# Performance work log

Measured on AMD Instinct MI355X. Metric: run time of the kernel, lower is better.

The kernel has to match this reference:

```python
import jax, jax.numpy as jnp
import numpy as np

T = 8192  # context/question length (input_shape[2])
D = 128   # feature dim (input_shape[3])


def setup_inputs() -> dict:
    key = jax.random.key(0)
    k1, k2 = jax.random.split(key)
    x = jax.random.normal(k1, (2, 1, T, D), dtype=jnp.float32)
    kernel = jax.random.normal(k2, (3 * D,), dtype=jnp.float32)
    return {"x": x, "kernel": kernel}


def reference(x, kernel):
    context = x[0, 0]   # (T, D)
    question = x[1, 0]  # (T, D)
    w_c, w_q, w_m = kernel[:D], kernel[D:2 * D], kernel[2 * D:]

    # Additive similarity: S[i,j] = c_i.w_c + q_j.w_q + (c_i*q_j).w_m
    # Avoids materializing the (T, T, 3D) tiled/concatenated tensor.
    S = (context @ w_c)[:, None] + (question @ w_q)[None, :] \
        + (context * w_m) @ question.T  # (T, T)

    A = jax.nn.softmax(S, axis=-1)  # row-wise softmax, as tf.nn.softmax on 2D

    # C2Q attention: U_A[i] = sum_j A[i,j] * q_j
    U_A = A @ question  # (T, D)

    # Q2C attention: b = row-max of A, h = sum_i b_i * c_i, tiled over rows
    b = jnp.max(A, axis=1)          # (T,)
    h = b @ context                 # (D,)
    H_A = jnp.broadcast_to(h, (T, D))

    # megamerge: [c, U_A, c*U_A, c*H_A]
    G = jnp.concatenate([context, U_A, context * U_A, context * H_A], axis=-1)
    return G  # (T, 4D)
```

## Files before the change

### kernel.cpp

```cpp
#include <hip/hip_runtime.h>
#include <hip/hip_bf16.h>

#define T 8192
#define D 128
#define NSPLIT 8
#define JLEN (T / NSPLIT)
#define BN 64
#define NITER (JLEN / BN)
#define BM 128
#define LOG2E 1.44269504088896f

typedef _Float16 half4_t __attribute__((ext_vector_type(4)));
typedef _Float16 half8_t __attribute__((ext_vector_type(8)));
typedef float floatx4 __attribute__((ext_vector_type(4)));

__global__ void prep_kernel(const float* __restrict__ x, const float* __restrict__ kern,
                            _Float16* __restrict__ q16, _Float16* __restrict__ qT16,
                            _Float16* __restrict__ cm16, float* __restrict__ qq2) {
    const float* context  = x;
    const float* question = x + (size_t)T * D;
    const float* wq = kern + D;
    const float* wm = kern + 2 * D;
    __shared__ __align__(16) _Float16 tile[32][136];
    int j0 = blockIdx.x * 32;
    int t = threadIdx.x;
    int c4 = t & 31;
    int rsub = t >> 5;
    float4 wqv = ((const float4*)wq)[c4];
    float4 wmv = ((const float4*)wm)[c4];
    for (int p = 0; p < 4; ++p) {
        int row = p * 8 + rsub;
        float4 q = ((const float4*)(question + (size_t)(j0 + row) * D))[c4];
        float4 c = ((const float4*)(context  + (size_t)(j0 + row) * D))[c4];
        half4_t qh;
        qh[0] = (_Float16)q.x; qh[1] = (_Float16)q.y; qh[2] = (_Float16)q.z; qh[3] = (_Float16)q.w;
        *(half4_t*)(q16 + (size_t)(j0 + row) * D + c4 * 4) = qh;
        *(half4_t*)&tile[row][c4 * 4] = qh;
        half4_t ch;
        ch[0] = (_Float16)(c.x * wmv.x * LOG2E); ch[1] = (_Float16)(c.y * wmv.y * LOG2E);
        ch[2] = (_Float16)(c.z * wmv.z * LOG2E); ch[3] = (_Float16)(c.w * wmv.w * LOG2E);
        *(half4_t*)(cm16 + (size_t)(j0 + row) * D + c4 * 4) = ch;
        float s = q.x * wqv.x + q.y * wqv.y + q.z * wqv.z + q.w * wqv.w;
        for (int dx = 1; dx <= 16; dx <<= 1) s += __shfl_xor(s, dx);
        if (c4 == 0) qq2[j0 + row] = s * LOG2E;
    }
    __syncthreads();
    for (int p = 0; p < 2; ++p) {
        int chunk = t + p * 256;
        int d = chunk >> 2, jo = (chunk & 3) * 8;
        half8_t v;
        for (int s2 = 0; s2 < 8; ++s2) v[s2] = tile[jo + s2][d];
        *(half8_t*)(qT16 + (size_t)d * T + j0 + jo) = v;
    }
}

__global__ __launch_bounds__(256, 2)
void flash_kernel(const _Float16* __restrict__ q16, const _Float16* __restrict__ qT16,
                  const _Float16* __restrict__ cm16, const float* __restrict__ qq2,
                  unsigned char* __restrict__ Opart, float* __restrict__ mpart,
                  float* __restrict__ lpart) {
    __shared__ __align__(16) _Float16 Kt[64][144];
    __shared__ __align__(16) _Float16 Vt[128][72];
    __shared__ __align__(16) float qqs[JLEN];

    int bx = blockIdx.x;
    int rb = bx >> 3;
    int sp = bx & 7;
    int tid = threadIdx.x;
    int wave = tid >> 6;
    int lane = tid & 63;
    int quad = lane >> 4;
    int l15 = lane & 15;
    int rbase = rb * BM + wave * 32;

    ((float4*)qqs)[tid] = ((const float4*)(qq2 + (size_t)sp * JLEN))[tid];

    half8_t qfrag[2][4];
    for (int mt = 0; mt < 2; ++mt)
        for (int ks = 0; ks < 4; ++ks)
            qfrag[mt][ks] = *(const half8_t*)(cm16 + (size_t)(rbase + mt * 16 + l15) * D
                                              + ks * 32 + quad * 8);

    floatx4 acc[2][8];
    for (int mt = 0; mt < 2; ++mt)
        for (int nt = 0; nt < 8; ++nt)
            for (int r = 0; r < 4; ++r) acc[mt][nt][r] = 0.f;
    float m_run[2] = {-INFINITY, -INFINITY};
    float l_run[2] = {0.f, 0.f};

    half8_t kreg[4], vreg[4];
    {
        int j0 = sp * JLEN;
        for (int k = 0; k < 4; ++k) {
            int idx = tid + k * 256;
            kreg[k] = *(const half8_t*)(q16 + (size_t)(j0 + (idx >> 4)) * D + (idx & 15) * 8);
            vreg[k] = *(const half8_t*)(qT16 + (size_t)(idx >> 3) * T + j0 + (idx & 7) * 8);
        }
    }

    for (int it = 0; it < NITER; ++it) {
        for (int k = 0; k < 4; ++k) {
            int idx = tid + k * 256;
            *(half8_t*)&Kt[idx >> 4][(idx & 15) * 8] = kreg[k];
        }
        for (int k = 0; k < 4; ++k) {
            int idx = tid + k * 256;
            int dr = idx >> 3, c8 = idx & 7;
            int ph0 = (c8 >> 2) * 32 + (c8 & 1) * 16 + ((c8 >> 1) & 1) * 4;
            half4_t lo, hi;
            lo[0] = vreg[k][0]; lo[1] = vreg[k][1]; lo[2] = vreg[k][2]; lo[3] = vreg[k][3];
            hi[0] = vreg[k][4]; hi[1] = vreg[k][5]; hi[2] = vreg[k][6]; hi[3] = vreg[k][7];
            *(half4_t*)&Vt[dr][ph0]     = lo;
            *(half4_t*)&Vt[dr][ph0 + 8] = hi;
        }
        __syncthreads();

        if (it + 1 < NITER) {
            int j0n = sp * JLEN + (it + 1) * BN;
            for (int k = 0; k < 4; ++k) {
                int idx = tid + k * 256;
                kreg[k] = *(const half8_t*)(q16 + (size_t)(j0n + (idx >> 4)) * D + (idx & 15) * 8);
                vreg[k] = *(const half8_t*)(qT16 + (size_t)(idx >> 3) * T + j0n + (idx & 7) * 8);
            }
        }

        floatx4 St[2][4];
        for (int jt = 0; jt < 4; ++jt) {
            float4 bias = *(const float4*)&qqs[it * 64 + jt * 16 + quad * 4];
            St[0][jt][0] = bias.x; St[0][jt][1] = bias.y; St[0][jt][2] = bias.z; St[0][jt][3] = bias.w;
            St[1][jt][0] = bias.x; St[1][jt][1] = bias.y; St[1][jt][2] = bias.z; St[1][jt][3] = bias.w;
        }
        for (int ks = 0; ks < 4; ++ks)
            for (int jt = 0; jt < 4; ++jt) {
                half8_t a = *(const half8_t*)&Kt[jt * 16 + l15][ks * 32 + quad * 8];
                St[0][jt] = __builtin_amdgcn_mfma_f32_16x16x32_f16(a, qfrag[0][ks], St[0][jt], 0, 0, 0);
                St[1][jt] = __builtin_amdgcn_mfma_f32_16x16x32_f16(a, qfrag[1][ks], St[1][jt], 0, 0, 0);
            }

        half4_t apv[2][4];
        float alpha[2];
        for (int mt = 0; mt < 2; ++mt) {
            float mx = St[mt][0][0];
            for (int jt = 0; jt < 4; ++jt)
                for (int r = 0; r < 4; ++r) mx = fmaxf(mx, St[mt][jt][r]);
            mx = fmaxf(mx, __shfl_xor(mx, 16));
            mx = fmaxf(mx, __shfl_xor(mx, 32));
            float mnew = fmaxf(m_run[mt], mx);
            alpha[mt] = __builtin_amdgcn_exp2f(m_run[mt] - mnew);
            m_run[mt] = mnew;
            float ps = 0.f;
            for (int jt = 0; jt < 4; ++jt) {
                float p0 = __builtin_amdgcn_exp2f(St[mt][jt][0] - mnew);
                float p1 = __builtin_amdgcn_exp2f(St[mt][jt][1] - mnew);
                float p2 = __builtin_amdgcn_exp2f(St[mt][jt][2] - mnew);
                float p3 = __builtin_amdgcn_exp2f(St[mt][jt][3] - mnew);
                ps += (p0 + p1) + (p2 + p3);
                apv[mt][jt][0] = (_Float16)p0;
                apv[mt][jt][1] = (_Float16)p1;
                apv[mt][jt][2] = (_Float16)p2;
                apv[mt][jt][3] = (_Float16)p3;
            }
            ps += __shfl_xor(ps, 16);
            ps += __shfl_xor(ps, 32);
            l_run[mt] = l_run[mt] * alpha[mt] + ps;
        }
        for (int mt = 0; mt < 2; ++mt) {
            float aT[4];
            for (int r = 0; r < 4; ++r)
                aT[r] = __shfl(alpha[mt], quad * 4 + r);
            for (int nt = 0; nt < 8; ++nt)
                for (int r = 0; r < 4; ++r) acc[mt][nt][r] *= aT[r];
        }

        for (int pr = 0; pr < 2; ++pr) {
            for (int nt = 0; nt < 8; ++nt) {
                half8_t bb = *(const half8_t*)&Vt[nt * 16 + l15][pr * 32 + quad * 8];
                half4_t b0, b1;
                b0[0] = bb[0]; b0[1] = bb[1]; b0[2] = bb[2]; b0[3] = bb[3];
                b1[0] = bb[4]; b1[1] = bb[5]; b1[2] = bb[6]; b1[3] = bb[7];
                int jt0 = pr * 2, jt1 = pr * 2 + 1;
                acc[0][nt] = __builtin_amdgcn_mfma_f32_16x16x16f16(apv[0][jt0], b0, acc[0][nt], 0, 0, 0);
                acc[1][nt] = __builtin_amdgcn_mfma_f32_16x16x16f16(apv[1][jt0], b0, acc[1][nt], 0, 0, 0);
                acc[0][nt] = __builtin_amdgcn_mfma_f32_16x16x16f16(apv[0][jt1], b1, acc[0][nt], 0, 0, 0);
                acc[1][nt] = __builtin_amdgcn_mfma_f32_16x16x16f16(apv[1][jt1], b1, acc[1][nt], 0, 0, 0);
            }
        }
        __syncthreads();
    }

    for (int mt = 0; mt < 2; ++mt) {
        if (quad == 0) {
            int iq = rbase + mt * 16 + l15;
            mpart[(size_t)sp * T + iq] = m_run[mt];
            lpart[(size_t)sp * T + iq] = l_run[mt];
        }
        float rinv[4];
        for (int r = 0; r < 4; ++r)
            rinv[r] = 1.0f / __shfl(l_run[mt], quad * 4 + r);
        int i = rbase + mt * 16 + quad * 4;
        for (int nt = 0; nt < 4; ++nt)
            ;
        for (int nt = 0; nt < 8; ++nt) {
            for (int r = 0; r < 4; r += 2) {
                float v0 = acc[mt][nt][r]     * rinv[r];
                float v1 = acc[mt][nt][r + 1] * rinv[r + 1];
                int p0 = __builtin_amdgcn_cvt_pk_fp8_f32(v0, v0, 0, false);
                int p1 = __builtin_amdgcn_cvt_pk_fp8_f32(v1, v1, 0, false);
                Opart[((size_t)sp * T + (i + r))     * D + nt * 16 + l15] = (unsigned char)(p0 & 0xFF);
                Opart[((size_t)sp * T + (i + r + 1)) * D + nt * 16 + l15] = (unsigned char)(p1 & 0xFF);
            }
        }
    }
}

__global__ void merge_kernel(const unsigned char* __restrict__ Opart, const float* __restrict__ mpart,
                             const float* __restrict__ lpart, float* __restrict__ U_A,
                             float* __restrict__ linv) {
    int t = threadIdx.x;
    int i = blockIdx.x * 16 + (t >> 4);
    int c = t & 15;
    float mp[NSPLIT];
    float mstar = -INFINITY;
    for (int sp = 0; sp < NSPLIT; ++sp) {
        mp[sp] = mpart[(size_t)sp * T + i];
        mstar = fmaxf(mstar, mp[sp]);
    }
    float L = 0.f;
    float u[8];
    for (int k = 0; k < 8; ++k) u[k] = 0.f;
    int d0 = c * 8;
    for (int sp = 0; sp < NSPLIT; ++sp) {
        float w = __builtin_amdgcn_exp2f(mp[sp] - mstar) * lpart[(size_t)sp * T + i];
        L += w;
        uint2 ow = *(const uint2*)(Opart + ((size_t)sp * T + i) * D + d0);
        u[0] += __builtin_amdgcn_cvt_f32_fp8(ow.x, 0) * w;
        u[1] += __builtin_amdgcn_cvt_f32_fp8(ow.x, 1) * w;
        u[2] += __builtin_amdgcn_cvt_f32_fp8(ow.x, 2) * w;
        u[3] += __builtin_amdgcn_cvt_f32_fp8(ow.x, 3) * w;
        u[4] += __builtin_amdgcn_cvt_f32_fp8(ow.y, 0) * w;
        u[5] += __builtin_amdgcn_cvt_f32_fp8(ow.y, 1) * w;
        u[6] += __builtin_amdgcn_cvt_f32_fp8(ow.y, 2) * w;
        u[7] += __builtin_amdgcn_cvt_f32_fp8(ow.y, 3) * w;
    }
    float invL = 1.0f / L;
    float4 s0 = make_float4(u[0] * invL, u[1] * invL, u[2] * invL, u[3] * invL);
    float4 s1 = make_float4(u[4] * invL, u[5] * invL, u[6] * invL, u[7] * invL);
    *(float4*)(U_A + (size_t)i * D + d0) = s0;
    *(float4*)(U_A + (size_t)i * D + d0 + 4) = s1;
    if (c == 0) linv[i] = invL;
}

__global__ void hsum_part_kernel(const float* __restrict__ x, const float* __restrict__ linv,
                                 float* __restrict__ hpart) {
    const float* context = x;
    int t = threadIdx.x;
    int d = t & 127, g = t >> 7;
    int i0 = blockIdx.x * 128 + g * 64;
    float s = 0.f;
    for (int k = 0; k < 64; ++k)
        s += context[(size_t)(i0 + k) * D + d] * linv[i0 + k];
    hpart[(size_t)(blockIdx.x * 2 + g) * 128 + d] = s;
}

__global__ void hreduce_kernel(const float* __restrict__ hpart, float* __restrict__ h) {
    int d = threadIdx.x;
    float s = 0.f;
    for (int k = 0; k < 128; ++k) s += hpart[(size_t)k * 128 + d];
    h[d] = s;
}

__global__ void assemble_kernel(const float* __restrict__ x, const float* __restrict__ U_A,
                                const float* __restrict__ h, float* __restrict__ out) {
    const float* context = x;
    int gid = blockIdx.x * 256 + threadIdx.x;
    int base = gid * 4;
    int i = base >> 9;
    int c = base & 511;
    int seg = c >> 7, d = c & 127;
    float4 r;
    if (seg == 0) {
        r = *(const float4*)(context + (size_t)i * D + d);
    } else if (seg == 1) {
        r = *(const float4*)(U_A + (size_t)i * D + d);
    } else if (seg == 2) {
        float4 a = *(const float4*)(context + (size_t)i * D + d);
        float4 b = *(const float4*)(U_A + (size_t)i * D + d);
        r = make_float4(a.x * b.x, a.y * b.y, a.z * b.z, a.w * b.w);
    } else {
        float4 a = *(const float4*)(context + (size_t)i * D + d);
        float4 b = *(const float4*)(h + d);
        r = make_float4(a.x * b.x, a.y * b.y, a.z * b.z, a.w * b.w);
    }
    *(float4*)(out + base) = r;
}

extern "C" void kernel_launch(void* const* d_in, const int* in_sizes, int n_in,
                              void* d_out, int out_size, void* d_ws, size_t ws_size,
                              hipStream_t stream) {
    const float* x = (const float*)d_in[0];
    const float* kern = (const float*)d_in[1];
    float* out = (float*)d_out;

    char* w = (char*)d_ws;
    size_t off = 0;
    _Float16* q16  = (_Float16*)(w + off); off += (size_t)T * D * 2;
    _Float16* qT16 = (_Float16*)(w + off); off += (size_t)T * D * 2;
    _Float16* cm16 = (_Float16*)(w + off); off += (size_t)T * D * 2;
    float* qq2   = (float*)(w + off); off += (size_t)T * 4;
    float* mpart = (float*)(w + off); off += (size_t)NSPLIT * T * 4;
    float* lpart = (float*)(w + off); off += (size_t)NSPLIT * T * 4;
    float* U_A   = (float*)(w + off); off += (size_t)T * D * 4;
    float* linv  = (float*)(w + off); off += (size_t)T * 4;
    float* hpart = (float*)(w + off); off += (size_t)128 * 128 * 4;
    float* h     = (float*)(w + off); off += (size_t)D * 4;

    unsigned char* Opart = (unsigned char*)d_out;

    prep_kernel<<<256, 256, 0, stream>>>(x, kern, q16, qT16, cm16, qq2);
    flash_kernel<<<512, 256, 0, stream>>>(q16, qT16, cm16, qq2, Opart, mpart, lpart);
    merge_kernel<<<512, 256, 0, stream>>>(Opart, mpart, lpart, U_A, linv);
    hsum_part_kernel<<<64, 256, 0, stream>>>(x, linv, hpart);
    hreduce_kernel<<<1, 128, 0, stream>>>(hpart, h);
    assemble_kernel<<<4096, 256, 0, stream>>>(x, U_A, h, out);
}
```

Before: 131.7 us.

## Rework flash kernel with 32x32 MFMA, double-buffered LDS, and fused reduction kernels

The flash attention kernel moves from 16x16 MFMA tiles to 32x32x16 MFMA with one 32-row tile per wave. K and V now sit in double-buffered LDS with an XOR-style swizzle for V, prefetched two iterations ahead, so there is one barrier per iteration. It also adds lazy rescaling (skipped when no row max grows), packed fp16 conversion and setprio hints. On the host side, the h reduction is restructured: a new combine kernel computes the inverse softmax normalisers straight from the per-split m and l values, and merge folds in the final h reduce, cutting one launch. The risk is more register pressure from the 16-wide accumulators and mistakes in the new lane mapping.

```diff
diff --git a/kernel.cpp b/kernel.cpp
--- a/kernel.cpp
+++ b/kernel.cpp
@@ -10,9 +10,12 @@
 #define BM 128
 #define LOG2E 1.44269504088896f
 
+typedef _Float16 half2_t __attribute__((ext_vector_type(2)));
 typedef _Float16 half4_t __attribute__((ext_vector_type(4)));
 typedef _Float16 half8_t __attribute__((ext_vector_type(8)));
+typedef __fp16 fp16x2_t __attribute__((ext_vector_type(2)));
 typedef float floatx4 __attribute__((ext_vector_type(4)));
+typedef float floatx16 __attribute__((ext_vector_type(16)));
 
 __global__ void prep_kernel(const float* __restrict__ x, const float* __restrict__ kern,
                             _Float16* __restrict__ q16, _Float16* __restrict__ qT16,
@@ -59,164 +62,207 @@
                   const _Float16* __restrict__ cm16, const float* __restrict__ qq2,
                   unsigned char* __restrict__ Opart, float* __restrict__ mpart,
                   float* __restrict__ lpart) {
-    __shared__ __align__(16) _Float16 Kt[64][144];
-    __shared__ __align__(16) _Float16 Vt[128][72];
+    __shared__ __align__(16) _Float16 Kt[2][64][136];
+    __shared__ __align__(16) _Float16 Vt[2][128][64];
     __shared__ __align__(16) float qqs[JLEN];
 
-    int bx = blockIdx.x;
-    int rb = bx >> 3;
-    int sp = bx & 7;
-    int tid = threadIdx.x;
-    int wave = tid >> 6;
-    int lane = tid & 63;
-    int quad = lane >> 4;
-    int l15 = lane & 15;
-    int rbase = rb * BM + wave * 32;
+    const int bx = blockIdx.x;
+    const int rb = bx >> 3;
+    const int sp = bx & 7;
+    const int tid = threadIdx.x;
+    const int wave = tid >> 6;
+    const int lane = tid & 63;
+    const int l31 = lane & 31;
+    const int h = lane >> 5;
+    const int rbase = rb * BM + wave * 32;
+    const int q = rbase + l31;
+    const int sig = (l31 & 19) | ((l31 & 4) << 1) | ((l31 & 8) >> 1);
 
     ((float4*)qqs)[tid] = ((const float4*)(qq2 + (size_t)sp * JLEN))[tid];
 
-    half8_t qfrag[2][4];
-    for (int mt = 0; mt < 2; ++mt)
-        for (int ks = 0; ks < 4; ++ks)
-            qfrag[mt][ks] = *(const half8_t*)(cm16 + (size_t)(rbase + mt * 16 + l15) * D
-                                              + ks * 32 + quad * 8);
-
-    floatx4 acc[2][8];
-    for (int mt = 0; mt < 2; ++mt)
-        for (int nt = 0; nt < 8; ++nt)
-            for (int r = 0; r < 4; ++r) acc[mt][nt][r] = 0.f;
-    float m_run[2] = {-INFINITY, -INFINITY};
-    float l_run[2] = {0.f, 0.f};
-
+    half8_t qfrag[8];
+#pragma unroll
+    for (int ks = 0; ks < 8; ++ks)
+        qfrag[ks] = *(const half8_t*)(cm16 + (size_t)q * D + ks * 16 + h * 8);
+
+    floatx16 acc[4];
+#pragma unroll
+    for (int nt = 0; nt < 4; ++nt)
+#pragma unroll
+        for (int r = 0; r < 16; ++r) acc[nt][r] = 0.f;
+    float m_run = -INFINITY, l_run = 0.f;
+
+    const int j0 = sp * JLEN;
     half8_t kreg[4], vreg[4];
-    {
-        int j0 = sp * JLEN;
-        for (int k = 0; k < 4; ++k) {
-            int idx = tid + k * 256;
-            kreg[k] = *(const half8_t*)(q16 + (size_t)(j0 + (idx >> 4)) * D + (idx & 15) * 8);
-            vreg[k] = *(const half8_t*)(qT16 + (size_t)(idx >> 3) * T + j0 + (idx & 7) * 8);
-        }
-    }
+#pragma unroll
+    for (int k = 0; k < 4; ++k) {
+        int idx = tid + k * 256;
+        kreg[k] = *(const half8_t*)(q16 + (size_t)(j0 + (idx >> 4)) * D + (idx & 15) * 8);
+        vreg[k] = *(const half8_t*)(qT16 + (size_t)(idx >> 3) * T + j0 + (idx & 7) * 8);
+    }
+#pragma unroll
+    for (int k = 0; k < 4; ++k) {
+        int idx = tid + k * 256;
+        *(half8_t*)&Kt[0][idx >> 4][(idx & 15) * 8] = kreg[k];
+        int dr = idx >> 3, c8 = idx & 7;
+        *(half8_t*)&Vt[0][dr][((c8 + (dr & 7)) & 7) * 8] = vreg[k];
+    }
+#pragma unroll
+    for (int k = 0; k < 4; ++k) {
+        int idx = tid + k * 256;
+        kreg[k] = *(const half8_t*)(q16 + (size_t)(j0 + BN + (idx >> 4)) * D + (idx & 15) * 8);
+        vreg[k] = *(const half8_t*)(qT16 + (size_t)(idx >> 3) * T + j0 + BN + (idx & 7) * 8);
+    }
+    __syncthreads();
 
     for (int it = 0; it < NITER; ++it) {
-        for (int k = 0; k < 4; ++k) {
-            int idx = tid + k * 256;
-            *(half8_t*)&Kt[idx >> 4][(idx & 15) * 8] = kreg[k];
-        }
-        for (int k = 0; k < 4; ++k) {
-            int idx = tid + k * 256;
-            int dr = idx >> 3, c8 = idx & 7;
-            int ph0 = (c8 >> 2) * 32 + (c8 & 1) * 16 + ((c8 >> 1) & 1) * 4;
-            half4_t lo, hi;
-            lo[0] = vreg[k][0]; lo[1] = vreg[k][1]; lo[2] = vreg[k][2]; lo[3] = vreg[k][3];
-            hi[0] = vreg[k][4]; hi[1] = vreg[k][5]; hi[2] = vreg[k][6]; hi[3] = vreg[k][7];
-            *(half4_t*)&Vt[dr][ph0]     = lo;
-            *(half4_t*)&Vt[dr][ph0 + 8] = hi;
-        }
-        __syncthreads();
-
+        const int cur = it & 1;
         if (it + 1 < NITER) {
-            int j0n = sp * JLEN + (it + 1) * BN;
+#pragma unroll
             for (int k = 0; k < 4; ++k) {
                 int idx = tid + k * 256;
-                kreg[k] = *(const half8_t*)(q16 + (size_t)(j0n + (idx >> 4)) * D + (idx & 15) * 8);
-                vreg[k] = *(const half8_t*)(qT16 + (size_t)(idx >> 3) * T + j0n + (idx & 7) * 8);
-            }
-        }
-
-        floatx4 St[2][4];
-        for (int jt = 0; jt < 4; ++jt) {
-            float4 bias = *(const float4*)&qqs[it * 64 + jt * 16 + quad * 4];
-            St[0][jt][0] = bias.x; St[0][jt][1] = bias.y; St[0][jt][2] = bias.z; St[0][jt][3] = bias.w;
-            St[1][jt][0] = bias.x; St[1][jt][1] = bias.y; St[1][jt][2] = bias.z; St[1][jt][3] = bias.w;
-        }
-        for (int ks = 0; ks < 4; ++ks)
-            for (int jt = 0; jt < 4; ++jt) {
-                half8_t a = *(const half8_t*)&Kt[jt * 16 + l15][ks * 32 + quad * 8];
-                St[0][jt] = __builtin_amdgcn_mfma_f32_16x16x32_f16(a, qfrag[0][ks], St[0][jt], 0, 0, 0);
-                St[1][jt] = __builtin_amdgcn_mfma_f32_16x16x32_f16(a, qfrag[1][ks], St[1][jt], 0, 0, 0);
-            }
-
-        half4_t apv[2][4];
-        float alpha[2];
-        for (int mt = 0; mt < 2; ++mt) {
-            float mx = St[mt][0][0];
-            for (int jt = 0; jt < 4; ++jt)
-                for (int r = 0; r < 4; ++r) mx = fmaxf(mx, St[mt][jt][r]);
-            mx = fmaxf(mx, __shfl_xor(mx, 16));
-            mx = fmaxf(mx, __shfl_xor(mx, 32));
-            float mnew = fmaxf(m_run[mt], mx);
-            alpha[mt] = __builtin_amdgcn_exp2f(m_run[mt] - mnew);
-            m_run[mt] = mnew;
-            float ps = 0.f;
-            for (int jt = 0; jt < 4; ++jt) {
-                float p0 = __builtin_amdgcn_exp2f(St[mt][jt][0] - mnew);
-                float p1 = __builtin_amdgcn_exp2f(St[mt][jt][1] - mnew);
-                float p2 = __builtin_amdgcn_exp2f(St[mt][jt][2] - mnew);
-                float p3 = __builtin_amdgcn_exp2f(St[mt][jt][3] - mnew);
-                ps += (p0 + p1) + (p2 + p3);
-                apv[mt][jt][0] = (_Float16)p0;
-                apv[mt][jt][1] = (_Float16)p1;
-                apv[mt][jt][2] = (_Float16)p2;
-                apv[mt][jt][3] = (_Float16)p3;
-            }
-            ps += __shfl_xor(ps, 16);
-            ps += __shfl_xor(ps, 32);
-            l_run[mt] = l_run[mt] * alpha[mt] + ps;
-        }
-        for (int mt = 0; mt < 2; ++mt) {
-            float aT[4];
-            for (int r = 0; r < 4; ++r)
-                aT[r] = __shfl(alpha[mt], quad * 4 + r);
-            for (int nt = 0; nt < 8; ++nt)
-                for (int r = 0; r < 4; ++r) acc[mt][nt][r] *= aT[r];
-        }
-
-        for (int pr = 0; pr < 2; ++pr) {
-            for (int nt = 0; nt < 8; ++nt) {
-                half8_t bb = *(const half8_t*)&Vt[nt * 16 + l15][pr * 32 + quad * 8];
-                half4_t b0, b1;
-                b0[0] = bb[0]; b0[1] = bb[1]; b0[2] = bb[2]; b0[3] = bb[3];
-                b1[0] = bb[4]; b1[1] = bb[5]; b1[2] = bb[6]; b1[3] = bb[7];
-                int jt0 = pr * 2, jt1 = pr * 2 + 1;
-                acc[0][nt] = __builtin_amdgcn_mfma_f32_16x16x16f16(apv[0][jt0], b0, acc[0][nt], 0, 0, 0);
-                acc[1][nt] = __builtin_amdgcn_mfma_f32_16x16x16f16(apv[1][jt0], b0, acc[1][nt], 0, 0, 0);
-                acc[0][nt] = __builtin_amdgcn_mfma_f32_16x16x16f16(apv[0][jt1], b1, acc[0][nt], 0, 0, 0);
-                acc[1][nt] = __builtin_amdgcn_mfma_f32_16x16x16f16(apv[1][jt1], b1, acc[1][nt], 0, 0, 0);
-            }
-        }
+                *(half8_t*)&Kt[cur ^ 1][idx >> 4][(idx & 15) * 8] = kreg[k];
+                int dr = idx >> 3, c8 = idx & 7;
+                *(half8_t*)&Vt[cur ^ 1][dr][((c8 + (dr & 7)) & 7) * 8] = vreg[k];
+            }
+        }
+        if (it + 2 < NITER) {
+            int jn = j0 + (it + 2) * BN;
+#pragma unroll
+            for (int k = 0; k < 4; ++k) {
+                int idx = tid + k * 256;
+                kreg[k] = *(const half8_t*)(q16 + (size_t)(jn + (idx >> 4)) * D + (idx & 15) * 8);
+                vreg[k] = *(const half8_t*)(qT16 + (size_t)(idx >> 3) * T + jn + (idx & 7) * 8);
+            }
+        }
+
+        floatx16 St[2];
+#pragma unroll
+        for (int jt = 0; jt < 2; ++jt) {
+            const float* qb = &qqs[it * 64 + jt * 32];
+            float4 b0 = *(const float4*)(qb + 8 * h);
+            float4 b1 = *(const float4*)(qb + 4 + 8 * h);
+            float4 b2 = *(const float4*)(qb + 16 + 8 * h);
+            float4 b3 = *(const float4*)(qb + 20 + 8 * h);
+            St[jt][0]  = b0.x; St[jt][1]  = b0.y; St[jt][2]  = b0.z; St[jt][3]  = b0.w;
+            St[jt][4]  = b1.x; St[jt][5]  = b1.y; St[jt][6]  = b1.z; St[jt][7]  = b1.w;
+            St[jt][8]  = b2.x; St[jt][9]  = b2.y; St[jt][10] = b2.z; St[jt][11] = b2.w;
+            St[jt][12] = b3.x; St[jt][13] = b3.y; St[jt][14] = b3.z; St[jt][15] = b3.w;
+            __builtin_amdgcn_s_setprio(1);
+#pragma unroll
+            for (int ks = 0; ks < 8; ++ks) {
+                half8_t a = *(const half8_t*)&Kt[cur][jt * 32 + sig][ks * 16 + h * 8];
+                St[jt] = __builtin_amdgcn_mfma_f32_32x32x16_f16(a, qfrag[ks], St[jt], 0, 0, 0);
+            }
+            __builtin_amdgcn_s_setprio(0);
+        }
+
+        float mx = St[0][0];
+#pragma unroll
+        for (int r = 1; r < 16; ++r) mx = fmaxf(mx, St[0][r]);
+#pragma unroll
+        for (int r = 0; r < 16; ++r) mx = fmaxf(mx, St[1][r]);
+        mx = fmaxf(mx, __shfl_xor(mx, 32));
+        if (__any(mx > m_run)) {
+            float mnew = fmaxf(m_run, mx);
+            float alpha = __builtin_amdgcn_exp2f(m_run - mnew);
+#pragma unroll
+            for (int nt = 0; nt < 4; ++nt)
+#pragma unroll
+                for (int r = 0; r < 16; ++r) acc[nt][r] *= alpha;
+            l_run *= alpha;
+            m_run = mnew;
+        }
+        half2_t pp[2][8];
+        float ps = 0.f;
+#pragma unroll
+        for (int jt = 0; jt < 2; ++jt)
+#pragma unroll
+            for (int r2 = 0; r2 < 8; ++r2) {
+                float p0 = __builtin_amdgcn_exp2f(St[jt][2 * r2]     - m_run);
+                float p1 = __builtin_amdgcn_exp2f(St[jt][2 * r2 + 1] - m_run);
+                ps += p0 + p1;
+                fp16x2_t pk = __builtin_amdgcn_cvt_pkrtz(p0, p1);
+                pp[jt][r2] = __builtin_bit_cast(half2_t, pk);
+            }
+        ps += __shfl_xor(ps, 32);
+        l_run += ps;
+
+        __builtin_amdgcn_s_setprio(1);
+#pragma unroll
+        for (int jt = 0; jt < 2; ++jt)
+#pragma unroll
+            for (int kb = 0; kb < 2; ++kb) {
+                half8_t pb;
+                pb[0] = pp[jt][kb * 4 + 0][0]; pb[1] = pp[jt][kb * 4 + 0][1];
+                pb[2] = pp[jt][kb * 4 + 1][0]; pb[3] = pp[jt][kb * 4 + 1][1];
+                pb[4] = pp[jt][kb * 4 + 2][0]; pb[5] = pp[jt][kb * 4 + 2][1];
+                pb[6] = pp[jt][kb * 4 + 3][0]; pb[7] = pp[jt][kb * 4 + 3][1];
+                const int pg = ((jt * 4 + kb * 2 + h) + (l31 & 7)) & 7;
+#pragma unroll
+                for (int nt = 0; nt < 4; ++nt) {
+                    half8_t va = *(const half8_t*)&Vt[cur][nt * 32 + l31][pg * 8];
+                    acc[nt] = __builtin_amdgcn_mfma_f32_32x32x16_f16(va, pb, acc[nt], 0, 0, 0);
+                }
+            }
+        __builtin_amdgcn_s_setprio(0);
         __syncthreads();
     }
 
-    for (int mt = 0; mt < 2; ++mt) {
-        if (quad == 0) {
-            int iq = rbase + mt * 16 + l15;
-            mpart[(size_t)sp * T + iq] = m_run[mt];
-            lpart[(size_t)sp * T + iq] = l_run[mt];
-        }
-        float rinv[4];
-        for (int r = 0; r < 4; ++r)
-            rinv[r] = 1.0f / __shfl(l_run[mt], quad * 4 + r);
-        int i = rbase + mt * 16 + quad * 4;
-        for (int nt = 0; nt < 4; ++nt)
-            ;
-        for (int nt = 0; nt < 8; ++nt) {
-            for (int r = 0; r < 4; r += 2) {
-                float v0 = acc[mt][nt][r]     * rinv[r];
-                float v1 = acc[mt][nt][r + 1] * rinv[r + 1];
-                int p0 = __builtin_amdgcn_cvt_pk_fp8_f32(v0, v0, 0, false);
-                int p1 = __builtin_amdgcn_cvt_pk_fp8_f32(v1, v1, 0, false);
-                Opart[((size_t)sp * T + (i + r))     * D + nt * 16 + l15] = (unsigned char)(p0 & 0xFF);
-                Opart[((size_t)sp * T + (i + r + 1)) * D + nt * 16 + l15] = (unsigned char)(p1 & 0xFF);
-            }
-        }
-    }
+    if (h == 0) {
+        mpart[(size_t)sp * T + q] = m_run;
+        lpart[(size_t)sp * T + q] = l_run;
+    }
+    float rinv = 1.0f / l_run;
+#pragma unroll
+    for (int nt = 0; nt < 4; ++nt)
+#pragma unroll
+        for (int rg = 0; rg < 4; ++rg) {
+            float v0 = acc[nt][rg * 4 + 0] * rinv;
+            float v1 = acc[nt][rg * 4 + 1] * rinv;
+            float v2 = acc[nt][rg * 4 + 2] * rinv;
+            float v3 = acc[nt][rg * 4 + 3] * rinv;
+            unsigned u = (unsigned)__builtin_amdgcn_cvt_pk_fp8_f32(v0, v1, 0, false);
+            u = (unsigned)__builtin_amdgcn_cvt_pk_fp8_f32(v2, v3, u, true);
+            *(unsigned*)(Opart + ((size_t)sp * T + q) * D + nt * 32 + rg * 8 + 4 * h) = u;
+        }
+}
+
+__global__ void combine_kernel(const float* __restrict__ x, const float* __restrict__ mpart,
+                               const float* __restrict__ lpart, float* __restrict__ hpart) {
+    __shared__ float linv_s[128];
+    int b = blockIdx.x, t = threadIdx.x;
+    if (t < 128) {
+        int i = b * 128 + t;
+        float mp[NSPLIT];
+        float mstar = -INFINITY;
+        for (int sp2 = 0; sp2 < NSPLIT; ++sp2) {
+            mp[sp2] = mpart[(size_t)sp2 * T + i];
+            mstar = fmaxf(mstar, mp[sp2]);
+        }
+        float L = 0.f;
+        for (int sp2 = 0; sp2 < NSPLIT; ++sp2)
+            L += __builtin_amdgcn_exp2f(mp[sp2] - mstar) * lpart[(size_t)sp2 * T + i];
+        linv_s[t] = 1.0f / L;
+    }
+    __syncthreads();
+    int d = t & 127, g = t >> 7;
+    int r0 = g * 64;
+    float s = 0.f;
+    for (int r = 0; r < 64; ++r)
+        s += x[(size_t)(b * 128 + r0 + r) * D + d] * linv_s[r0 + r];
+    hpart[(size_t)(b * 2 + g) * 128 + d] = s;
 }
 
 __global__ void merge_kernel(const unsigned char* __restrict__ Opart, const float* __restrict__ mpart,
                              const float* __restrict__ lpart, float* __restrict__ U_A,
-                             float* __restrict__ linv) {
+                             const float* __restrict__ hpart, float* __restrict__ h) {
     int t = threadIdx.x;
+    if (blockIdx.x == 0 && t < 128) {
+        float s = 0.f;
+        for (int k = 0; k < 128; ++k) s += hpart[(size_t)k * 128 + t];
+        h[t] = s;
+    }
     int i = blockIdx.x * 16 + (t >> 4);
     int c = t & 15;
     float mp[NSPLIT];
@@ -247,26 +293,6 @@
     float4 s1 = make_float4(u[4] * invL, u[5] * invL, u[6] * invL, u[7] * invL);
     *(float4*)(U_A + (size_t)i * D + d0) = s0;
     *(float4*)(U_A + (size_t)i * D + d0 + 4) = s1;
-    if (c == 0) linv[i] = invL;
-}
-
-__global__ void hsum_part_kernel(const float* __restrict__ x, const float* __restrict__ linv,
-                                 float* __restrict__ hpart) {
-    const float* context = x;
-    int t = threadIdx.x;
-    int d = t & 127, g = t >> 7;
-    int i0 = blockIdx.x * 128 + g * 64;
-    float s = 0.f;
-    for (int k = 0; k < 64; ++k)
-        s += context[(size_t)(i0 + k) * D + d] * linv[i0 + k];
-    hpart[(size_t)(blockIdx.x * 2 + g) * 128 + d] = s;
-}
-
-__global__ void hreduce_kernel(const float* __restrict__ hpart, float* __restrict__ h) {
-    int d = threadIdx.x;
-    float s = 0.f;
-    for (int k = 0; k < 128; ++k) s += hpart[(size_t)k * 128 + d];
-    h[d] = s;
 }
 
 __global__ void assemble_kernel(const float* __restrict__ x, const float* __restrict__ U_A,
@@ -310,7 +336,6 @@
     float* mpart = (float*)(w + off); off += (size_t)NSPLIT * T * 4;
     float* lpart = (float*)(w + off); off += (size_t)NSPLIT * T * 4;
     float* U_A   = (float*)(w + off); off += (size_t)T * D * 4;
-    float* linv  = (float*)(w + off); off += (size_t)T * 4;
     float* hpart = (float*)(w + off); off += (size_t)128 * 128 * 4;
     float* h     = (float*)(w + off); off += (size_t)D * 4;
 
@@ -318,8 +343,7 @@
 
     prep_kernel<<<256, 256, 0, stream>>>(x, kern, q16, qT16, cm16, qq2);
     flash_kernel<<<512, 256, 0, stream>>>(q16, qT16, cm16, qq2, Opart, mpart, lpart);
-    merge_kernel<<<512, 256, 0, stream>>>(Opart, mpart, lpart, U_A, linv);
-    hsum_part_kernel<<<64, 256, 0, stream>>>(x, linv, hpart);
-    hreduce_kernel<<<1, 128, 0, stream>>>(hpart, h);
+    combine_kernel<<<64, 256, 0, stream>>>(x, mpart, lpart, hpart);
+    merge_kernel<<<512, 256, 0, stream>>>(Opart, mpart, lpart, U_A, hpart, h);
     assemble_kernel<<<4096, 256, 0, stream>>>(x, U_A, h, out);
 }
```

After: 127.9 us. 1.03x faster.
